# Performance work log

Hardware: AMD Instinct MI355X
Metric: run time of the kernel (lower is better)

## Reference

```python
import jax, jax.numpy as jnp
import numpy as np

D = 256
N_EDGES = 8192
N_CORNERS = 4096


def setup_inputs() -> dict:
    key = jax.random.key(0)
    ks = jax.random.split(key, 8)
    scale = 1.0 / np.sqrt(D)
    return {
        "edge_pred": jax.random.uniform(ks[0], (N_EDGES,), dtype=jnp.float32),
        "edge_corner": jax.random.randint(ks[1], (N_EDGES, 2), 0, N_CORNERS, dtype=jnp.int64),
        "all_corners": jax.random.uniform(ks[2], (N_CORNERS, 2), dtype=jnp.float32),
        "edge_x": jax.random.normal(ks[3], (N_EDGES, D), dtype=jnp.float32),
        "image_x": jax.random.normal(ks[4], (1024,), dtype=jnp.float32),
        "W1": jax.random.normal(ks[5], (D, D), dtype=jnp.float32) * scale,
        "b1": jnp.zeros((D,), dtype=jnp.float32),
        "W2": jax.random.normal(ks[6], (D, D), dtype=jnp.float32) * scale,
        "b2": jnp.zeros((D,), dtype=jnp.float32),
        "W3": jax.random.normal(ks[7], (3 * D, D), dtype=jnp.float32) * scale,
        "b3": jnp.zeros((D,), dtype=jnp.float32),
    }


def _linear_block(x, W, b):
    # LinearBlock: Linear followed by ReLU
    return jax.nn.relu(x @ W + b)


def reference(edge_pred, edge_corner, all_corners, edge_x, image_x, W1, b1, W2, b2, W3, b3):
    # 'fully' branch of MPModule.forward. edge_pred/edge_corner/all_corners/image_x
    # are unused in this branch (kept for signature fidelity).
    e1 = _linear_block(edge_x, W1, b1)              # [N, D]
    # (e1.unsqueeze(1) * e1).mean(-1) == (e1 @ e1.T) / D   -> [N, N]
    sim1 = (e1 @ e1.T) / D
    e2 = _linear_block(edge_x, W2, b2)
    sim2 = (e2 @ e2.T) / D
    # (edge_x * sim.unsqueeze(-1)).sum(1) == sim @ edge_x  -> [N, D]
    agg1 = sim1 @ edge_x
    agg2 = sim2 @ edge_x
    cat = jnp.concatenate([edge_x, agg1, agg2], axis=-1)  # [N, 3D]
    out = _linear_block(cat, W3, b3)                      # [N, D]
    return out
```

## Files before the change

kernel.cpp:

```cpp
#include <hip/hip_runtime.h>

#define NE 8192
#define DD 256
#define NSPLIT 32

typedef __attribute__((ext_vector_type(8))) short short8;
typedef __attribute__((ext_vector_type(4))) short short4v;
typedef __attribute__((ext_vector_type(8))) __bf16 bf16x8;
typedef __attribute__((ext_vector_type(4))) float floatx4;

__device__ __forceinline__ unsigned short f2bf(float f) {
  union { float f; unsigned int i; } v; v.f = f;
  unsigned int r = v.i + 0x7fffu + ((v.i >> 16) & 1u);
  return (unsigned short)(r >> 16);
}

__device__ __forceinline__ float bf2f(unsigned short h) {
  union { unsigned int i; float f; } v; v.i = ((unsigned int)h) << 16;
  return v.f;
}

__device__ __forceinline__ floatx4 mfma_bf16(short8 a, short8 b, floatx4 c) {
  return __builtin_amdgcn_mfma_f32_16x16x32_bf16(
      __builtin_bit_cast(bf16x8, a), __builtin_bit_cast(bf16x8, b), c, 0, 0, 0);
}

__device__ __forceinline__ void tcvt_tile(float* ls,
                                          const float* __restrict__ src, int C,
                                          unsigned short* __restrict__ dst, int R,
                                          int r0, int c0, int tid) {
  const int rr = tid >> 4, c4 = (tid & 15) * 4;
#pragma unroll
  for (int k = 0; k < 4; ++k)
    *(floatx4*)&ls[(rr + k * 16) * 68 + c4] =
        *(const floatx4*)&src[(size_t)(r0 + rr + k * 16) * C + c0 + c4];
  __syncthreads();
  const int cc = tid >> 2, rb = (tid & 3) * 16;
  short8 o0, o1;
#pragma unroll
  for (int i = 0; i < 8; ++i) {
    o0[i] = (short)f2bf(ls[(rb + i) * 68 + cc]);
    o1[i] = (short)f2bf(ls[(rb + 8 + i) * 68 + cc]);
  }
  unsigned short* dp = &dst[(size_t)(c0 + cc) * R + r0 + rb];
  *(short8*)dp = o0;
  *(short8*)(dp + 8) = o1;
}

__global__ void cvt_all(const float* __restrict__ x, unsigned short* __restrict__ xb,
                        unsigned short* __restrict__ xT,
                        const float* __restrict__ W1, unsigned short* __restrict__ W1t,
                        const float* __restrict__ W2, unsigned short* __restrict__ W2t,
                        const float* __restrict__ W3, unsigned short* __restrict__ W3t0) {
  __shared__ float ls[64 * 68];
  const int b = blockIdx.x, tid = threadIdx.x;
  if (b < 512) {
    const int p = b & 7, k = b >> 3;
    const int r0 = (16 * p + (k >> 2)) * 64, c0 = (k & 3) * 64;
    const int rr = tid >> 4, c4 = (tid & 15) * 4;
#pragma unroll
    for (int kk = 0; kk < 4; ++kk) {
      floatx4 v = *(const floatx4*)&x[(size_t)(r0 + rr + kk * 16) * DD + c0 + c4];
      *(floatx4*)&ls[(rr + kk * 16) * 68 + c4] = v;
      short4v s;
#pragma unroll
      for (int c = 0; c < 4; ++c) s[c] = (short)f2bf(v[c]);
      *(short4v*)&xb[(size_t)(r0 + rr + kk * 16) * DD + c0 + c4] = s;
    }
    __syncthreads();
    const int cc = tid >> 2, rb = (tid & 3) * 16;
    short8 o0, o1;
#pragma unroll
    for (int i = 0; i < 8; ++i) {
      o0[i] = (short)f2bf(ls[(rb + i) * 68 + cc]);
      o1[i] = (short)f2bf(ls[(rb + 8 + i) * 68 + cc]);
    }
    unsigned short* dp = &xT[(size_t)(c0 + cc) * NE + r0 + rb];
    *(short8*)dp = o0;
    *(short8*)(dp + 8) = o1;
  } else {
    int t = b - 512;
    const float* src = (t < 16) ? W1 : ((t < 32) ? W2 : W3);
    unsigned short* dst = (t < 16) ? W1t : ((t < 32) ? W2t : W3t0);
    t &= 15;
    tcvt_tile(ls, src, DD, dst, DD, (t >> 2) * 64, (t & 3) * 64, tid);
  }
}

__global__ __launch_bounds__(256, 4)
void e_gemm(const unsigned short* __restrict__ xb,
            const unsigned short* __restrict__ W1t, const float* __restrict__ b1,
            const unsigned short* __restrict__ W2t, const float* __restrict__ b2,
            unsigned short* __restrict__ e1, unsigned short* __restrict__ e2,
            unsigned short* __restrict__ e1T, unsigned short* __restrict__ e2T)
{
  __shared__ __align__(16) unsigned short smB1[64 * 136];
  __shared__ __align__(16) unsigned short smB2[64 * 136];
  const int T = threadIdx.x, lane = T & 63, wv = T >> 6;
  const int q = lane >> 4, r = lane & 15;
  const int L = blockIdx.x;
  const int p = L & 7, k = L >> 3;
  const int col0 = (k & 3) * 64, row0 = (16 * p + (k >> 2)) * 64;
  const unsigned short* Arow = &xb[(size_t)(row0 + wv * 16 + r) * DD + q * 8];

  floatx4 acc1[4], acc2[4];
#pragma unroll
  for (int j = 0; j < 4; ++j) {
    acc1[j] = (floatx4){0.f, 0.f, 0.f, 0.f};
    acc2[j] = (floatx4){0.f, 0.f, 0.f, 0.f};
  }

  short8 pb1[4], pb2[4];
#pragma unroll
  for (int pp = 0; pp < 4; ++pp) {
    const int id = pp * 256 + T, rr = id >> 4, k8 = (id & 15) * 8;
    pb1[pp] = *(const short8*)&W1t[(size_t)(col0 + rr) * DD + k8];
    pb2[pp] = *(const short8*)&W2t[(size_t)(col0 + rr) * DD + k8];
  }

  for (int kc = 0; kc < 256; kc += 128) {
#pragma unroll
    for (int pp = 0; pp < 4; ++pp) {
      const int id = pp * 256 + T, rr = id >> 4, k8 = (id & 15) * 8;
      *(short8*)&smB1[rr * 136 + k8] = pb1[pp];
      *(short8*)&smB2[rr * 136 + k8] = pb2[pp];
    }
    __syncthreads();
    short8 af[4];
#pragma unroll
    for (int ks = 0; ks < 4; ++ks)
      af[ks] = *(const short8*)&Arow[kc + ks * 32];
    if (kc + 128 < 256) {
#pragma unroll
      for (int pp = 0; pp < 4; ++pp) {
        const int id = pp * 256 + T, rr = id >> 4, k8 = (id & 15) * 8;
        pb1[pp] = *(const short8*)&W1t[(size_t)(col0 + rr) * DD + kc + 128 + k8];
        pb2[pp] = *(const short8*)&W2t[(size_t)(col0 + rr) * DD + kc + 128 + k8];
      }
    }
#pragma unroll
    for (int ks = 0; ks < 4; ++ks) {
#pragma unroll
      for (int j = 0; j < 4; ++j) {
        short8 b1f = *(const short8*)&smB1[(j * 16 + r) * 136 + ks * 32 + q * 8];
        short8 b2f = *(const short8*)&smB2[(j * 16 + r) * 136 + ks * 32 + q * 8];
        acc1[j] = mfma_bf16(af[ks], b1f, acc1[j]);
        acc2[j] = mfma_bf16(af[ks], b2f, acc2[j]);
      }
    }
    __syncthreads();
  }

  unsigned short* t1s = smB1;
  unsigned short* t2s = smB2;
#pragma unroll
  for (int j = 0; j < 4; ++j) {
    const int col = col0 + j * 16 + r;
    const int lc = j * 16 + r;
    const int lr = wv * 16 + q * 4;
    const int rowb = row0 + lr;
    const float b1v = b1[col], b2v = b2[col];
#pragma unroll
    for (int t = 0; t < 4; ++t) {
      unsigned short h1 = f2bf(fmaxf(acc1[j][t] + b1v, 0.0f));
      unsigned short h2 = f2bf(fmaxf(acc2[j][t] + b2v, 0.0f));
      t1s[lc * 68 + lr + t] = h1;
      t2s[lc * 68 + lr + t] = h2;
      e1[(size_t)(rowb + t) * DD + col] = h1;
      e2[(size_t)(rowb + t) * DD + col] = h2;
    }
  }
  __syncthreads();
  {
    const int c = T >> 2, seg = (T & 3) * 16;
    short8 v1a = *(short8*)&t1s[c * 68 + seg];
    short8 v1b = *(short8*)&t1s[c * 68 + seg + 8];
    short8 v2a = *(short8*)&t2s[c * 68 + seg];
    short8 v2b = *(short8*)&t2s[c * 68 + seg + 8];
    unsigned short* d1 = &e1T[(size_t)(col0 + c) * NE + row0 + seg];
    unsigned short* d2 = &e2T[(size_t)(col0 + c) * NE + row0 + seg];
    *(short8*)d1 = v1a; *(short8*)(d1 + 8) = v1b;
    *(short8*)d2 = v2a; *(short8*)(d2 + 8) = v2b;
  }
}

__global__ __launch_bounds__(256, 5)
void atb(const unsigned short* __restrict__ e1T, const unsigned short* __restrict__ e2T,
         const unsigned short* __restrict__ xT, unsigned short* __restrict__ P_T)
{
  __shared__ __align__(16) unsigned short smX[64 * 136];
  const int T = threadIdx.x, lane = T & 63, wv = T >> 6;
  const int q = lane >> 4, r = lane & 15;
  const int L = blockIdx.x;
  const int p = L & 7, k = L >> 3;
  const int mn = k >> 2;
  const int y = 4 * p + (k & 3);
  const int m0 = (mn >> 2) * 64, n0 = (mn & 3) * 64;
  const int j0 = y * (NE / NSPLIT);
  const unsigned short* E1row = &e1T[(size_t)(m0 + wv * 16 + r) * NE + j0 + q * 8];
  const unsigned short* E2row = &e2T[(size_t)(m0 + wv * 16 + r) * NE + j0 + q * 8];

  floatx4 acc1[4], acc2[4];
#pragma unroll
  for (int j = 0; j < 4; ++j) {
    acc1[j] = (floatx4){0.f, 0.f, 0.f, 0.f};
    acc2[j] = (floatx4){0.f, 0.f, 0.f, 0.f};
  }

  short8 px[4];
#pragma unroll
  for (int pp = 0; pp < 4; ++pp) {
    const int id = pp * 256 + T, mm = id >> 4, j8 = (id & 15) * 8;
    px[pp] = *(const short8*)&xT[(size_t)(n0 + mm) * NE + j0 + j8];
  }

  for (int jc = 0; jc < NE / NSPLIT; jc += 128) {
#pragma unroll
    for (int pp = 0; pp < 4; ++pp) {
      const int id = pp * 256 + T, mm = id >> 4, j8 = (id & 15) * 8;
      *(short8*)&smX[mm * 136 + j8] = px[pp];
    }
    __syncthreads();
    short8 a1[4], a2[4];
#pragma unroll
    for (int ks = 0; ks < 4; ++ks) {
      a1[ks] = *(const short8*)&E1row[jc + ks * 32];
      a2[ks] = *(const short8*)&E2row[jc + ks * 32];
    }
    if (jc + 128 < NE / NSPLIT) {
#pragma unroll
      for (int pp = 0; pp < 4; ++pp) {
        const int id = pp * 256 + T, mm = id >> 4, j8 = (id & 15) * 8;
        px[pp] = *(const short8*)&xT[(size_t)(n0 + mm) * NE + j0 + jc + 128 + j8];
      }
    }
#pragma unroll
    for (int ks = 0; ks < 4; ++ks) {
#pragma unroll
      for (int j = 0; j < 4; ++j) {
        short8 bx = *(const short8*)&smX[(j * 16 + r) * 136 + ks * 32 + q * 8];
        acc1[j] = mfma_bf16(a1[ks], bx, acc1[j]);
        acc2[j] = mfma_bf16(a2[ks], bx, acc2[j]);
      }
    }
    __syncthreads();
  }

#pragma unroll
  for (int j = 0; j < 4; ++j) {
    const int n = n0 + j * 16 + r;
    const int m = m0 + wv * 16 + q * 4;
    short4v s1, s2;
#pragma unroll
    for (int t = 0; t < 4; ++t) {
      s1[t] = (short)f2bf(acc1[j][t]);
      s2[t] = (short)f2bf(acc2[j][t]);
    }
    *(short4v*)&P_T[(size_t)y * 65536 + n * DD + m] = s1;
    *(short4v*)&P_T[(size_t)(NSPLIT + y) * 65536 + n * DD + m] = s2;
  }
}

__global__ void reduce_g(const unsigned short* __restrict__ P_T, float* __restrict__ G_T) {
  int idx = blockIdx.x * 256 + threadIdx.x;
  int z = idx >> 14, off = (idx & 16383) * 4;
  floatx4 s = (floatx4){0.f, 0.f, 0.f, 0.f};
#pragma unroll
  for (int y = 0; y < NSPLIT; ++y) {
    short4v v = *(const short4v*)&P_T[(size_t)(z * NSPLIT + y) * 65536 + off];
#pragma unroll
    for (int c = 0; c < 4; ++c) s[c] += bf2f((unsigned short)v[c]);
  }
  *(floatx4*)&G_T[(size_t)z * 65536 + off] = s;
}

__global__ __launch_bounds__(256, 2)
void h_mfma(const float* __restrict__ G_T, const float* __restrict__ W3,
            unsigned short* __restrict__ H1t, unsigned short* __restrict__ H2t)
{
  __shared__ __align__(16) unsigned short smA[64 * 136];
  __shared__ __align__(16) unsigned short smB[64 * 136];
  const int T = threadIdx.x, lane = T & 63, wv = T >> 6;
  const int q = lane >> 4, r = lane & 15;
  const int z = blockIdx.z;
  const int me0 = (blockIdx.x >> 2) * 64, m30 = (blockIdx.x & 3) * 64;
  const float* G = G_T + (size_t)z * 65536;
  unsigned short* Ht = z ? H2t : H1t;
  const int woff = 256 + z * 256;

  floatx4 acc[4];
#pragma unroll
  for (int j = 0; j < 4; ++j) acc[j] = (floatx4){0.f, 0.f, 0.f, 0.f};

  for (int lc = 0; lc < 256; lc += 128) {
#pragma unroll
    for (int pp = 0; pp < 2; ++pp) {
      const int id = pp * 256 + T, lb = id >> 4, e4 = id & 15;
      floatx4 grow[4], wrow[4];
#pragma unroll
      for (int i = 0; i < 4; ++i) {
        grow[i] = *(const floatx4*)&G[(size_t)(lc + lb * 4 + i) * DD + me0 + e4 * 4];
        wrow[i] = *(const floatx4*)&W3[(size_t)(woff + lc + lb * 4 + i) * DD + m30 + e4 * 4];
      }
#pragma unroll
      for (int s4 = 0; s4 < 4; ++s4) {
        const int c = (s4 + e4) & 3;
        short4v ga = {(short)f2bf(grow[0][c] * 0.00390625f),
                      (short)f2bf(grow[1][c] * 0.00390625f),
                      (short)f2bf(grow[2][c] * 0.00390625f),
                      (short)f2bf(grow[3][c] * 0.00390625f)};
        short4v wa = {(short)f2bf(wrow[0][c]), (short)f2bf(wrow[1][c]),
                      (short)f2bf(wrow[2][c]), (short)f2bf(wrow[3][c])};
        *(short4v*)&smA[(e4 * 4 + c) * 136 + lb * 4] = ga;
        *(short4v*)&smB[(e4 * 4 + c) * 136 + lb * 4] = wa;
      }
    }
    __syncthreads();
#pragma unroll
    for (int ks = 0; ks < 4; ++ks) {
      short8 af = *(const short8*)&smA[(wv * 16 + r) * 136 + ks * 32 + q * 8];
#pragma unroll
      for (int j = 0; j < 4; ++j) {
        short8 bf = *(const short8*)&smB[(j * 16 + r) * 136 + ks * 32 + q * 8];
        acc[j] = mfma_bf16(af, bf, acc[j]);
      }
    }
    __syncthreads();
  }
#pragma unroll
  for (int j = 0; j < 4; ++j) {
    const int m3 = m30 + j * 16 + r;
    const int me = me0 + wv * 16 + q * 4;
    short4v v;
#pragma unroll
    for (int i = 0; i < 4; ++i) v[i] = (short)f2bf(acc[j][i]);
    *(short4v*)&Ht[(size_t)m3 * DD + me] = v;
  }
}

__global__ __launch_bounds__(256, 5)
void out_gemm(const unsigned short* __restrict__ xb,
              const unsigned short* __restrict__ e1, const unsigned short* __restrict__ e2,
              const unsigned short* __restrict__ W3t0,
              const unsigned short* __restrict__ H1t, const unsigned short* __restrict__ H2t,
              const float* __restrict__ b3, float* __restrict__ out)
{
  __shared__ __align__(16) unsigned short smB[64 * 136];
  const int T = threadIdx.x, lane = T & 63, wv = T >> 6;
  const int q = lane >> 4, r = lane & 15;
  const int L = blockIdx.x;
  const int p = L & 7, k = L >> 3;
  const int col0 = (k & 3) * 64, row0 = (16 * p + (k >> 2)) * 64;

  const unsigned short* As[3] = {xb, e1, e2};
  const unsigned short* Bs[3] = {W3t0, H1t, H2t};
  const size_t arow = (size_t)(row0 + wv * 16 + r) * DD + q * 8;

  floatx4 acc[4];
#pragma unroll
  for (int j = 0; j < 4; ++j) acc[j] = (floatx4){0.f, 0.f, 0.f, 0.f};

  short8 qb[4];
#pragma unroll
  for (int pp = 0; pp < 4; ++pp) {
    const int id = pp * 256 + T, rr = id >> 4, k8 = (id & 15) * 8;
    qb[pp] = *(const short8*)&Bs[0][(size_t)(col0 + rr) * DD + k8];
  }

  for (int rd = 0; rd < 6; ++rd) {
#pragma unroll
    for (int pp = 0; pp < 4; ++pp) {
      const int id = pp * 256 + T, rr = id >> 4, k8 = (id & 15) * 8;
      *(short8*)&smB[rr * 136 + k8] = qb[pp];
    }
    __syncthreads();
    const int kc = (rd & 1) * 128;
    const unsigned short* A = As[rd >> 1];
    short8 af[4];
#pragma unroll
    for (int ks = 0; ks < 4; ++ks)
      af[ks] = *(const short8*)&A[arow + kc + ks * 32];
    if (rd + 1 < 6) {
      const int s = (rd + 1) >> 1, kcn = ((rd + 1) & 1) * 128;
      const unsigned short* B = Bs[s];
#pragma unroll
      for (int pp = 0; pp < 4; ++pp) {
        const int id = pp * 256 + T, rr = id >> 4, k8 = (id & 15) * 8;
        qb[pp] = *(const short8*)&B[(size_t)(col0 + rr) * DD + kcn + k8];
      }
    }
#pragma unroll
    for (int ks = 0; ks < 4; ++ks) {
#pragma unroll
      for (int j = 0; j < 4; ++j) {
        short8 bf = *(const short8*)&smB[(j * 16 + r) * 136 + ks * 32 + q * 8];
        acc[j] = mfma_bf16(af[ks], bf, acc[j]);
      }
    }
    __syncthreads();
  }
#pragma unroll
  for (int j = 0; j < 4; ++j) {
    const int col = col0 + j * 16 + r;
    const float bv = b3[col];
    const int rowb = row0 + wv * 16 + q * 4;
#pragma unroll
    for (int t = 0; t < 4; ++t)
      out[(size_t)(rowb + t) * DD + col] = fmaxf(acc[j][t] + bv, 0.0f);
  }
}

extern "C" void kernel_launch(void* const* d_in, const int* in_sizes, int n_in,
                              void* d_out, int out_size, void* d_ws, size_t ws_size,
                              hipStream_t stream) {
  (void)in_sizes; (void)n_in; (void)out_size; (void)ws_size;
  const float* x  = (const float*)d_in[3];
  const float* W1 = (const float*)d_in[5];
  const float* b1 = (const float*)d_in[6];
  const float* W2 = (const float*)d_in[7];
  const float* b2 = (const float*)d_in[8];
  const float* W3 = (const float*)d_in[9];
  const float* b3 = (const float*)d_in[10];
  float* out = (float*)d_out;

  char* ws = (char*)d_ws;
  const size_t MB = 1u << 20;
  const size_t KB = 1u << 10;
  unsigned short* xb   = (unsigned short*)ws;
  unsigned short* xT   = (unsigned short*)(ws + 4 * MB);
  unsigned short* e1   = (unsigned short*)(ws + 8 * MB);
  unsigned short* e2   = (unsigned short*)(ws + 12 * MB);
  unsigned short* e1T  = (unsigned short*)(ws + 16 * MB);
  unsigned short* e2T  = (unsigned short*)(ws + 20 * MB);
  unsigned short* W1t  = (unsigned short*)(ws + 24 * MB);
  unsigned short* W2t  = (unsigned short*)(ws + 24 * MB + 128 * KB);
  unsigned short* W3t0 = (unsigned short*)(ws + 24 * MB + 256 * KB);
  unsigned short* H1t  = (unsigned short*)(ws + 24 * MB + 384 * KB);
  unsigned short* H2t  = (unsigned short*)(ws + 24 * MB + 512 * KB);
  float* G_T           = (float*)(ws + 24 * MB + 640 * KB);
  unsigned short* P_T  = (unsigned short*)(ws + 25 * MB);

  cvt_all<<<560, 256, 0, stream>>>(x, xb, xT, W1, W1t, W2, W2t, W3, W3t0);
  e_gemm<<<512, 256, 0, stream>>>(xb, W1t, b1, W2t, b2, e1, e2, e1T, e2T);
  atb<<<512, 256, 0, stream>>>(e1T, e2T, xT, P_T);
  reduce_g<<<128, 256, 0, stream>>>(P_T, G_T);
  h_mfma<<<dim3(16, 1, 2), 256, 0, stream>>>(G_T, W3, H1t, H2t);
  out_gemm<<<512, 256, 0, stream>>>(xb, e1, e2, W3t0, H1t, H2t, b3, out);
}
```

Baseline: 122.0 us.

## Stage full 256-wide K tiles in XOR-swizzled LDS for three GEMM kernels

The e_gemm, atb and out_gemm kernels now load the whole 256-element K slice of the B operand into shared memory at once, replacing two 128-wide chunks and removing one barrier round per chunk. The padded 136-stride layout is replaced by a 512-byte row with an XOR swizzle to avoid LDS bank conflicts. Shared memory per block roughly doubles and more A fragments sit in registers, so launch-bound occupancy targets are lowered, which reduces latency hiding.

```diff
diff --git a/kernel.cpp b/kernel.cpp
--- a/kernel.cpp
+++ b/kernel.cpp
@@ -23,6 +23,13 @@
 __device__ __forceinline__ floatx4 mfma_bf16(short8 a, short8 b, floatx4 c) {
   return __builtin_amdgcn_mfma_f32_16x16x32_bf16(
       __builtin_bit_cast(bf16x8, a), __builtin_bit_cast(bf16x8, b), c, 0, 0, 0);
+}
+
+__device__ __forceinline__ unsigned short* swzp(unsigned short* base, int row, int byteoff) {
+  return (unsigned short*)((char*)base + row * 512 + (byteoff ^ ((row & 7) << 4)));
+}
+__device__ __forceinline__ const unsigned short* swzc(const unsigned short* base, int row, int byteoff) {
+  return (const unsigned short*)((const char*)base + row * 512 + (byteoff ^ ((row & 7) << 4)));
 }
 
 __device__ __forceinline__ void tcvt_tile(float* ls,
@@ -87,15 +94,15 @@
   }
 }
 
-__global__ __launch_bounds__(256, 4)
+__global__ __launch_bounds__(256, 2)
 void e_gemm(const unsigned short* __restrict__ xb,
             const unsigned short* __restrict__ W1t, const float* __restrict__ b1,
             const unsigned short* __restrict__ W2t, const float* __restrict__ b2,
             unsigned short* __restrict__ e1, unsigned short* __restrict__ e2,
             unsigned short* __restrict__ e1T, unsigned short* __restrict__ e2T)
 {
-  __shared__ __align__(16) unsigned short smB1[64 * 136];
-  __shared__ __align__(16) unsigned short smB2[64 * 136];
+  __shared__ __align__(16) unsigned short smB1[64 * 256];
+  __shared__ __align__(16) unsigned short smB2[64 * 256];
   const int T = threadIdx.x, lane = T & 63, wv = T >> 6;
   const int q = lane >> 4, r = lane & 15;
   const int L = blockIdx.x;
@@ -110,46 +117,30 @@
     acc2[j] = (floatx4){0.f, 0.f, 0.f, 0.f};
   }
 
-  short8 pb1[4], pb2[4];
-#pragma unroll
-  for (int pp = 0; pp < 4; ++pp) {
-    const int id = pp * 256 + T, rr = id >> 4, k8 = (id & 15) * 8;
-    pb1[pp] = *(const short8*)&W1t[(size_t)(col0 + rr) * DD + k8];
-    pb2[pp] = *(const short8*)&W2t[(size_t)(col0 + rr) * DD + k8];
-  }
-
-  for (int kc = 0; kc < 256; kc += 128) {
-#pragma unroll
-    for (int pp = 0; pp < 4; ++pp) {
-      const int id = pp * 256 + T, rr = id >> 4, k8 = (id & 15) * 8;
-      *(short8*)&smB1[rr * 136 + k8] = pb1[pp];
-      *(short8*)&smB2[rr * 136 + k8] = pb2[pp];
-    }
-    __syncthreads();
-    short8 af[4];
-#pragma unroll
-    for (int ks = 0; ks < 4; ++ks)
-      af[ks] = *(const short8*)&Arow[kc + ks * 32];
-    if (kc + 128 < 256) {
-#pragma unroll
-      for (int pp = 0; pp < 4; ++pp) {
-        const int id = pp * 256 + T, rr = id >> 4, k8 = (id & 15) * 8;
-        pb1[pp] = *(const short8*)&W1t[(size_t)(col0 + rr) * DD + kc + 128 + k8];
-        pb2[pp] = *(const short8*)&W2t[(size_t)(col0 + rr) * DD + kc + 128 + k8];
-      }
-    }
-#pragma unroll
-    for (int ks = 0; ks < 4; ++ks) {
-#pragma unroll
-      for (int j = 0; j < 4; ++j) {
-        short8 b1f = *(const short8*)&smB1[(j * 16 + r) * 136 + ks * 32 + q * 8];
-        short8 b2f = *(const short8*)&smB2[(j * 16 + r) * 136 + ks * 32 + q * 8];
-        acc1[j] = mfma_bf16(af[ks], b1f, acc1[j]);
-        acc2[j] = mfma_bf16(af[ks], b2f, acc2[j]);
-      }
-    }
-    __syncthreads();
-  }
+#pragma unroll
+  for (int pp = 0; pp < 8; ++pp) {
+    const int id = pp * 256 + T, rr = id >> 5, c8 = (id & 31) * 8;
+    *(short8*)swzp(smB1, rr, (id & 31) * 16) =
+        *(const short8*)&W1t[(size_t)(col0 + rr) * DD + c8];
+    *(short8*)swzp(smB2, rr, (id & 31) * 16) =
+        *(const short8*)&W2t[(size_t)(col0 + rr) * DD + c8];
+  }
+  short8 af[8];
+#pragma unroll
+  for (int ks = 0; ks < 8; ++ks) af[ks] = *(const short8*)&Arow[ks * 32];
+  __syncthreads();
+
+#pragma unroll
+  for (int ks = 0; ks < 8; ++ks) {
+#pragma unroll
+    for (int j = 0; j < 4; ++j) {
+      short8 b1f = *(const short8*)swzc(smB1, j * 16 + r, ks * 64 + q * 16);
+      short8 b2f = *(const short8*)swzc(smB2, j * 16 + r, ks * 64 + q * 16);
+      acc1[j] = mfma_bf16(af[ks], b1f, acc1[j]);
+      acc2[j] = mfma_bf16(af[ks], b2f, acc2[j]);
+    }
+  }
+  __syncthreads();
 
   unsigned short* t1s = smB1;
   unsigned short* t2s = smB2;
@@ -184,11 +175,11 @@
   }
 }
 
-__global__ __launch_bounds__(256, 5)
+__global__ __launch_bounds__(256, 4)
 void atb(const unsigned short* __restrict__ e1T, const unsigned short* __restrict__ e2T,
          const unsigned short* __restrict__ xT, unsigned short* __restrict__ P_T)
 {
-  __shared__ __align__(16) unsigned short smX[64 * 136];
+  __shared__ __align__(16) unsigned short smX[64 * 256];
   const int T = threadIdx.x, lane = T & 63, wv = T >> 6;
   const int q = lane >> 4, r = lane & 15;
   const int L = blockIdx.x;
@@ -207,43 +198,28 @@
     acc2[j] = (floatx4){0.f, 0.f, 0.f, 0.f};
   }
 
-  short8 px[4];
-#pragma unroll
-  for (int pp = 0; pp < 4; ++pp) {
-    const int id = pp * 256 + T, mm = id >> 4, j8 = (id & 15) * 8;
-    px[pp] = *(const short8*)&xT[(size_t)(n0 + mm) * NE + j0 + j8];
-  }
-
-  for (int jc = 0; jc < NE / NSPLIT; jc += 128) {
-#pragma unroll
-    for (int pp = 0; pp < 4; ++pp) {
-      const int id = pp * 256 + T, mm = id >> 4, j8 = (id & 15) * 8;
-      *(short8*)&smX[mm * 136 + j8] = px[pp];
-    }
-    __syncthreads();
-    short8 a1[4], a2[4];
-#pragma unroll
-    for (int ks = 0; ks < 4; ++ks) {
-      a1[ks] = *(const short8*)&E1row[jc + ks * 32];
-      a2[ks] = *(const short8*)&E2row[jc + ks * 32];
-    }
-    if (jc + 128 < NE / NSPLIT) {
-#pragma unroll
-      for (int pp = 0; pp < 4; ++pp) {
-        const int id = pp * 256 + T, mm = id >> 4, j8 = (id & 15) * 8;
-        px[pp] = *(const short8*)&xT[(size_t)(n0 + mm) * NE + j0 + jc + 128 + j8];
-      }
-    }
-#pragma unroll
-    for (int ks = 0; ks < 4; ++ks) {
-#pragma unroll
-      for (int j = 0; j < 4; ++j) {
-        short8 bx = *(const short8*)&smX[(j * 16 + r) * 136 + ks * 32 + q * 8];
-        acc1[j] = mfma_bf16(a1[ks], bx, acc1[j]);
-        acc2[j] = mfma_bf16(a2[ks], bx, acc2[j]);
-      }
-    }
-    __syncthreads();
+#pragma unroll
+  for (int pp = 0; pp < 8; ++pp) {
+    const int id = pp * 256 + T, mm = id >> 5, c8 = (id & 31) * 8;
+    *(short8*)swzp(smX, mm, (id & 31) * 16) =
+        *(const short8*)&xT[(size_t)(n0 + mm) * NE + j0 + c8];
+  }
+  short8 a1[8], a2[8];
+#pragma unroll
+  for (int ks = 0; ks < 8; ++ks) {
+    a1[ks] = *(const short8*)&E1row[ks * 32];
+    a2[ks] = *(const short8*)&E2row[ks * 32];
+  }
+  __syncthreads();
+
+#pragma unroll
+  for (int ks = 0; ks < 8; ++ks) {
+#pragma unroll
+    for (int j = 0; j < 4; ++j) {
+      short8 bx = *(const short8*)swzc(smX, j * 16 + r, ks * 64 + q * 16);
+      acc1[j] = mfma_bf16(a1[ks], bx, acc1[j]);
+      acc2[j] = mfma_bf16(a2[ks], bx, acc2[j]);
+    }
   }
 
 #pragma unroll
@@ -338,14 +314,14 @@
   }
 }
 
-__global__ __launch_bounds__(256, 5)
+__global__ __launch_bounds__(256, 4)
 void out_gemm(const unsigned short* __restrict__ xb,
               const unsigned short* __restrict__ e1, const unsigned short* __restrict__ e2,
               const unsigned short* __restrict__ W3t0,
               const unsigned short* __restrict__ H1t, const unsigned short* __restrict__ H2t,
               const float* __restrict__ b3, float* __restrict__ out)
 {
-  __shared__ __align__(16) unsigned short smB[64 * 136];
+  __shared__ __align__(16) unsigned short smB[64 * 256];
   const int T = threadIdx.x, lane = T & 63, wv = T >> 6;
   const int q = lane >> 4, r = lane & 15;
   const int L = blockIdx.x;
@@ -360,40 +336,38 @@
 #pragma unroll
   for (int j = 0; j < 4; ++j) acc[j] = (floatx4){0.f, 0.f, 0.f, 0.f};
 
-  short8 qb[4];
-#pragma unroll
-  for (int pp = 0; pp < 4; ++pp) {
-    const int id = pp * 256 + T, rr = id >> 4, k8 = (id & 15) * 8;
-    qb[pp] = *(const short8*)&Bs[0][(size_t)(col0 + rr) * DD + k8];
-  }
-
-  for (int rd = 0; rd < 6; ++rd) {
-#pragma unroll
-    for (int pp = 0; pp < 4; ++pp) {
-      const int id = pp * 256 + T, rr = id >> 4, k8 = (id & 15) * 8;
-      *(short8*)&smB[rr * 136 + k8] = qb[pp];
+  short8 qb[8];
+#pragma unroll
+  for (int pp = 0; pp < 8; ++pp) {
+    const int id = pp * 256 + T, rr = id >> 5, c8 = (id & 31) * 8;
+    qb[pp] = *(const short8*)&Bs[0][(size_t)(col0 + rr) * DD + c8];
+  }
+
+#pragma unroll 1
+  for (int s = 0; s < 3; ++s) {
+#pragma unroll
+    for (int pp = 0; pp < 8; ++pp) {
+      const int id = pp * 256 + T, rr = id >> 5;
+      *(short8*)swzp(smB, rr, (id & 31) * 16) = qb[pp];
     }
     __syncthreads();
-    const int kc = (rd & 1) * 128;
-    const unsigned short* A = As[rd >> 1];
-    short8 af[4];
-#pragma unroll
-    for (int ks = 0; ks < 4; ++ks)
-      af[ks] = *(const short8*)&A[arow + kc + ks * 32];
-    if (rd + 1 < 6) {
-      const int s = (rd + 1) >> 1, kcn = ((rd + 1) & 1) * 128;
-      const unsigned short* B = Bs[s];
-#pragma unroll
-      for (int pp = 0; pp < 4; ++pp) {
-        const int id = pp * 256 + T, rr = id >> 4, k8 = (id & 15) * 8;
-        qb[pp] = *(const short8*)&B[(size_t)(col0 + rr) * DD + kcn + k8];
+    const unsigned short* A = As[s];
+    short8 af[8];
+#pragma unroll
+    for (int ks = 0; ks < 8; ++ks) af[ks] = *(const short8*)&A[arow + ks * 32];
+    if (s + 1 < 3) {
+      const unsigned short* B = Bs[s + 1];
+#pragma unroll
+      for (int pp = 0; pp < 8; ++pp) {
+        const int id = pp * 256 + T, rr = id >> 5, c8 = (id & 31) * 8;
+        qb[pp] = *(const short8*)&B[(size_t)(col0 + rr) * DD + c8];
       }
     }
 #pragma unroll
-    for (int ks = 0; ks < 4; ++ks) {
+    for (int ks = 0; ks < 8; ++ks) {
 #pragma unroll
       for (int j = 0; j < 4; ++j) {
-        short8 bf = *(const short8*)&smB[(j * 16 + r) * 136 + ks * 32 + q * 8];
+        short8 bf = *(const short8*)swzc(smB, j * 16 + r, ks * 64 + q * 16);
         acc[j] = mfma_bf16(af[ks], bf, acc[j]);
       }
     }
```

Measured after the change: 123.7 us. About the same (+1.4%).
